# Kernel optimization log

Measured on AMD Instinct MI355X. Metric: run time of the kernel, lower is better.

## Reference

```python
import jax, jax.numpy as jnp
import numpy as np

NUM_GROUPS = 32
NUM_HEADS = 8
EPS = 1e-6


def group_norm(x, gamma, beta):
    B, C, H, W = x.shape
    xg = x.reshape(B, NUM_GROUPS, C // NUM_GROUPS, H, W)
    mean = xg.mean(axis=(2, 3, 4), keepdims=True)
    var = xg.var(axis=(2, 3, 4), keepdims=True)
    xn = (xg - mean) * jax.lax.rsqrt(var + EPS)
    xn = xn.reshape(B, C, H, W)
    return xn * gamma[None, :, None, None] + beta[None, :, None, None]


def setup_inputs() -> dict:
    key = jax.random.key(0)
    ks = jax.random.split(key, 3)
    B, C, H, W = 8, 512, 32, 32
    x = jax.random.normal(ks[0], (B, C, H, W), dtype=jnp.float32)
    # xavier_uniform for conv1x1: fan_in=C, fan_out per weight
    lim_qkv = float(np.sqrt(6.0 / (C + 3 * C)))
    w_qkv = jax.random.uniform(ks[1], (3 * C, C), minval=-lim_qkv, maxval=lim_qkv, dtype=jnp.float32)
    b_qkv = jnp.zeros((3 * C,), dtype=jnp.float32)
    lim_p = float(np.sqrt(6.0 / (C + C)))
    w_proj = jax.random.uniform(ks[2], (C, C), minval=-lim_p, maxval=lim_p, dtype=jnp.float32)
    b_proj = jnp.zeros((C,), dtype=jnp.float32)
    gamma = jnp.ones((C,), dtype=jnp.float32)
    beta = jnp.zeros((C,), dtype=jnp.float32)
    return {"x": x, "gamma": gamma, "beta": beta, "w_qkv": w_qkv, "b_qkv": b_qkv,
            "w_proj": w_proj, "b_proj": b_proj}


def reference(x, gamma, beta, w_qkv, b_qkv, w_proj, b_proj):
    B, C, H, W = x.shape
    N = H * W
    hd = C // NUM_HEADS
    scale = hd ** -0.5

    x_norm = group_norm(x, gamma, beta)
    # conv1x1 == channel GEMM: (B,C,H,W) -> (B,3C,H,W)
    qkv = jnp.einsum('bchw,oc->bohw', x_norm, w_qkv) + b_qkv[None, :, None, None]
    qkv = qkv.reshape(B, 3, NUM_HEADS, hd, N).transpose(1, 0, 2, 4, 3)
    q, k, v = qkv[0], qkv[1], qkv[2]

    attn = jnp.einsum('bhnd,bhmd->bhnm', q, k) * scale
    attn = jax.nn.softmax(attn, axis=-1)
    out = jnp.einsum('bhnm,bhmd->bhnd', attn, v)

    out = out.transpose(0, 1, 3, 2).reshape(B, C, H, W)
    out = jnp.einsum('bchw,oc->bohw', out, w_proj) + b_proj[None, :, None, None]
    return x + out
```

## Files before the change

### kernel.cpp

```cpp
#include <hip/hip_runtime.h>

#define LOG2E 1.4426950408889634f

typedef short bf16x8 __attribute__((ext_vector_type(8)));
typedef short short4v __attribute__((ext_vector_type(4)));
typedef float f32x4 __attribute__((ext_vector_type(4)));
typedef _Float16 half4v __attribute__((ext_vector_type(4)));
typedef unsigned u32x4 __attribute__((ext_vector_type(4)));
typedef unsigned __attribute__((address_space(1))) u32g;
typedef unsigned __attribute__((address_space(3))) u32l;

#define MFMA16(a, b, c) __builtin_amdgcn_mfma_f32_16x16x32_bf16((a), (b), (c), 0, 0, 0)

__device__ __forceinline__ short f2bf(float f) {
  unsigned u = __builtin_bit_cast(unsigned, f);
  u += 0x7FFFu + ((u >> 16) & 1u);
  return (short)(u >> 16);
}

__device__ __forceinline__ unsigned cvtpk(float lo, float hi) {
  unsigned r;
  asm("v_cvt_pk_bf16_f32 %0, %1, %2" : "=v"(r) : "v"(lo), "v"(hi));
  return r;
}

__device__ __forceinline__ void g2l16(void* lds, const void* g) {
  __builtin_amdgcn_global_load_lds((u32g*)const_cast<void*>(g), (u32l*)lds, 16, 0, 0);
}

__global__ __launch_bounds__(256) void gn_kernel(const float* __restrict__ x,
                                                 const float* __restrict__ gamma,
                                                 const float* __restrict__ beta,
                                                 short* __restrict__ xn_t) {
  __shared__ _Float16 xs[16 * 1024];
  __shared__ float red[8];
  const int bg = blockIdx.x;
  const int b = bg >> 5, g = bg & 31;
  const int t = threadIdx.x;
  const float4* gx4 = (const float4*)(x + (size_t)(b * 512 + g * 16) * 1024);
  float s1 = 0.f, s2 = 0.f;
  for (int i = 0; i < 16; ++i) {
    float4 v = gx4[t + 256 * i];
    s1 += (v.x + v.y) + (v.z + v.w);
    s2 += (v.x * v.x + v.y * v.y) + (v.z * v.z + v.w * v.w);
    half4v pk = {(_Float16)v.x, (_Float16)v.y, (_Float16)v.z, (_Float16)v.w};
    *(half4v*)((char*)xs + i * 2048 + ((8 * t) ^ ((i & 7) << 4))) = pk;
  }
  for (int m = 1; m < 64; m <<= 1) {
    s1 += __shfl_xor(s1, m);
    s2 += __shfl_xor(s2, m);
  }
  if ((t & 63) == 0) {
    red[(t >> 6) * 2] = s1;
    red[(t >> 6) * 2 + 1] = s2;
  }
  __syncthreads();
  s1 = (red[0] + red[2]) + (red[4] + red[6]);
  s2 = (red[1] + red[3]) + (red[5] + red[7]);
  const float mean = s1 * (1.f / 16384.f);
  const float var = s2 * (1.f / 16384.f) - mean * mean;
  const float rstd = rsqrtf(var + 1e-6f);
  const int ci = t & 15;
  const float ga = gamma[g * 16 + ci] * rstd;
  const float be = beta[g * 16 + ci] - mean * ga;
  short* dst = xn_t + (size_t)b * 1024 * 512 + g * 16 + ci;
  const int sw = (ci & 7) << 4;
  for (int i = 0; i < 64; ++i) {
    int n = (t >> 4) + 16 * i;
    float v = (float)*(const _Float16*)((const char*)xs + ci * 2048 + ((2 * n) ^ sw));
    dst[(size_t)n * 512] = f2bf(fmaf(v, ga, be));
  }
}

__global__ __launch_bounds__(256) void f2bf2_kernel(const float* __restrict__ s1,
                                                    short* __restrict__ d1, int n1,
                                                    const float* __restrict__ s2,
                                                    short* __restrict__ d2) {
  int i = blockIdx.x * 256 + threadIdx.x;
  const float* s = (i < n1) ? s1 : s2;
  short* d = (i < n1) ? d1 : d2;
  int j = (i < n1) ? i : i - n1;
  float4 v = ((const float4*)s)[j];
  short4v o = {f2bf(v.x), f2bf(v.y), f2bf(v.z), f2bf(v.w)};
  *(short4v*)(d + (size_t)j * 4) = o;
}

__global__ __launch_bounds__(256) void qkv_gemm(const short* __restrict__ W,
                                                const short* __restrict__ xn,
                                                const float* __restrict__ bias,
                                                short* __restrict__ qbuf,
                                                short* __restrict__ kbuf,
                                                short* __restrict__ vtbuf) {
  __shared__ short a_sm[2][128 * 32];
  __shared__ short b_sm[2][128 * 32];
  const int t = threadIdx.x;
  const int lane = t & 63, w = t >> 6;
  const int nbase = blockIdx.x * 128;
  const int mbase = blockIdx.y * 128;
  const int b = blockIdx.z;
  const short* Asrc = W + (size_t)mbase * 512;
  const short* Bsrc = xn + (size_t)b * 1024 * 512 + (size_t)nbase * 512;

  const int j0 = t, j1 = t + 256;
  const int r0 = j0 >> 2, c0 = ((j0 & 3) ^ ((j0 >> 3) & 3)) * 8;
  const int r1 = j1 >> 2, c1 = ((j1 & 3) ^ ((j1 >> 3) & 3)) * 8;

#define STAGE(bi, kt)                                                 \
  {                                                                   \
    const int k0s = (kt) * 32;                                        \
    g2l16(&a_sm[bi][j0 * 8], Asrc + (size_t)r0 * 512 + k0s + c0);     \
    g2l16(&a_sm[bi][j1 * 8], Asrc + (size_t)r1 * 512 + k0s + c1);     \
    g2l16(&b_sm[bi][j0 * 8], Bsrc + (size_t)r0 * 512 + k0s + c0);     \
    g2l16(&b_sm[bi][j1 * 8], Bsrc + (size_t)r1 * 512 + k0s + c1);     \
  }

  const int wm = (w >> 1) * 64, wn = (w & 1) * 64;
  const int col = lane & 15, rg = lane >> 4;

  f32x4 acc[4][4] = {};

  STAGE(0, 0)
  __syncthreads();
  int cur = 0;

  for (int kt = 0; kt < 16; ++kt) {
    if (kt < 15) STAGE(cur ^ 1, kt + 1);
    bf16x8 af[4], bfr[4];
#pragma unroll
    for (int mf = 0; mf < 4; ++mf) {
      const int row = wm + mf * 16 + col;
      af[mf] = *(const bf16x8*)&a_sm[cur][row * 32 + ((rg ^ ((row >> 1) & 3)) * 8)];
    }
#pragma unroll
    for (int nf = 0; nf < 4; ++nf) {
      const int row = wn + nf * 16 + col;
      bfr[nf] = *(const bf16x8*)&b_sm[cur][row * 32 + ((rg ^ ((row >> 1) & 3)) * 8)];
    }
    __builtin_amdgcn_s_setprio(1);
#pragma unroll
    for (int mf = 0; mf < 4; ++mf)
#pragma unroll
      for (int nf = 0; nf < 4; ++nf)
        acc[mf][nf] = MFMA16(af[mf], bfr[nf], acc[mf][nf]);
    __builtin_amdgcn_s_setprio(0);
    __syncthreads();
    cur ^= 1;
  }
#undef STAGE

  const int section = mbase >> 9;
  for (int mf = 0; mf < 4; ++mf) {
    const int o0 = mbase + wm + mf * 16 + rg * 4;
    const int h = (o0 >> 6) & 7, d0 = o0 & 63;
    float b4[4];
    for (int r = 0; r < 4; ++r) b4[r] = bias[o0 + r];
    for (int nf = 0; nf < 4; ++nf) {
      const int n = nbase + wn + nf * 16 + col;
      if (section < 2) {
        short4v pkv;
        for (int r = 0; r < 4; ++r) pkv[r] = f2bf(acc[mf][nf][r] + b4[r]);
        short* dst = (section == 0) ? qbuf : kbuf;
        *(short4v*)&dst[((size_t)(b * 8 + h) * 1024 + n) * 64 + d0] = pkv;
      } else {
        for (int r = 0; r < 4; ++r)
          vtbuf[((size_t)(b * 8 + h) * 64 + d0 + r) * 1024 + n] =
              f2bf(acc[mf][nf][r] + b4[r]);
      }
    }
  }
}

__global__ __launch_bounds__(512, 4) void attn_kernel(const short* __restrict__ qbuf,
                                                      const short* __restrict__ kbuf,
                                                      const short* __restrict__ vtbuf,
                                                      short* __restrict__ ao) {
  __shared__ char smem[65536];
  const int t = threadIdx.x, lane = t & 63, w = t >> 6;
  const int col = lane & 15, rg = lane >> 4;
  const int grp = w >> 2, wq = w & 3;
  const int tg = t & 255;
  const int bh = blockIdx.x, qt = blockIdx.y;
  const int b = bh >> 3, h = bh & 7;
  const int qbase = qt * 128 + wq * 32;

  short* kb_ = (short*)(smem + grp * 32768);
  short* vb_ = (short*)(smem + grp * 32768 + 16384);

  bf16x8 aq[2][2];
  {
    const short* qp = qbuf + ((size_t)bh * 1024 + qbase) * 64;
#pragma unroll
    for (int mf = 0; mf < 2; ++mf)
#pragma unroll
      for (int kc = 0; kc < 2; ++kc)
        aq[mf][kc] = *(const bf16x8*)&qp[(mf * 16 + col) * 64 + kc * 32 + rg * 8];
  }

  const short* kp0 = kbuf + (size_t)bh * 65536 + grp * 32768;
  const short* vp0 = vtbuf + (size_t)bh * 65536 + grp * 512;

  uint4 kr[2], vr[2];
#define LOADK(kt)                                                                  \
  _Pragma("unroll") for (int i = 0; i < 2; ++i) {                                  \
    int j = tg + 256 * i;                                                          \
    kr[i] = *(const uint4*)&kp0[((size_t)(kt)*64 + (j >> 3)) * 64 + (j & 7) * 8];  \
  }
#define LOADV(kt)                                                                  \
  _Pragma("unroll") for (int i = 0; i < 2; ++i) {                                  \
    int j = tg + 256 * i;                                                          \
    vr[i] = *(const uint4*)&vp0[(size_t)(j >> 3) * 1024 + (kt)*64 + (j & 7) * 8];  \
  }
#define WRITEK(bi)                                                                 \
  _Pragma("unroll") for (int i = 0; i < 2; ++i) {                                  \
    int j = tg + 256 * i;                                                          \
    int row = j >> 3, off = j & 7;                                                 \
    *(uint4*)((char*)kb_ + (bi)*8192 + row * 128 + ((off * 16) ^ ((row & 7) << 4))) = kr[i]; \
  }
#define WRITEV(bi)                                                                 \
  _Pragma("unroll") for (int i = 0; i < 2; ++i) {                                  \
    int j = tg + 256 * i;                                                          \
    int d = j >> 3, g = j & 7;                                                     \
    int base = (g >> 2) * 64 + (g & 1) * 32 + ((g >> 1) & 1) * 8;                  \
    char* vb = (char*)vb_ + (bi)*8192 + d * 128;                                   \
    uint2 lo = {vr[i].x, vr[i].y}, hi = {vr[i].z, vr[i].w};                        \
    *(uint2*)(vb + ((base) ^ ((d & 7) << 4))) = lo;                                \
    *(uint2*)(vb + ((base + 16) ^ ((d & 7) << 4))) = hi;                           \
  }

  f32x4 oacc[2][4] = {};
  float mrun[2] = {-3e38f, -3e38f}, lrun[2] = {0.f, 0.f};
  const float kSL2E = 0.125f * LOG2E;
  int cur = 0;

  LOADK(0) LOADV(0) WRITEK(0) WRITEV(0)
  __syncthreads();

  for (int kt = 0; kt < 8; ++kt) {
    if (kt < 7) { LOADK(kt + 1) LOADV(kt + 1) }

    f32x4 sT[2][4];
    __builtin_amdgcn_s_setprio(1);
#pragma unroll
    for (int nf = 0; nf < 4; ++nf) {
      const int n = nf * 16 + col;
      const char* kb = (const char*)kb_ + cur * 8192 + n * 128;
      const int sw = (n & 7) << 4;
      bf16x8 bk0 = *(const bf16x8*)(kb + ((rg * 16) ^ sw));
      bf16x8 bk1 = *(const bf16x8*)(kb + ((64 + rg * 16) ^ sw));
#pragma unroll
      for (int mf = 0; mf < 2; ++mf) {
        f32x4 z = {};
        z = MFMA16(bk0, aq[mf][0], z);
        sT[mf][nf] = MFMA16(bk1, aq[mf][1], z);
      }
    }
    __builtin_amdgcn_s_setprio(0);

    unsigned pk[2][4][2];
#pragma unroll
    for (int mf = 0; mf < 2; ++mf) {
      f32x4 mv = sT[mf][0];
#pragma unroll
      for (int nf = 1; nf < 4; ++nf)
#pragma unroll
        for (int r = 0; r < 4; ++r) mv[r] = fmaxf(mv[r], sT[mf][nf][r]);
      float mx = fmaxf(fmaxf(mv[0], mv[1]), fmaxf(mv[2], mv[3]));
      if (!__all(mx * 0.125f <= mrun[mf] + 8.f)) {
        float mxr = fmaxf(mx, __shfl_xor(mx, 16));
        mxr = fmaxf(mxr, __shfl_xor(mxr, 32));
        const float pmax = mxr * 0.125f;
        const float mnew = fmaxf(mrun[mf], pmax);
        const float alpha = __builtin_amdgcn_exp2f((mrun[mf] - mnew) * LOG2E);
        mrun[mf] = mnew;
        lrun[mf] *= alpha;
#pragma unroll
        for (int df = 0; df < 4; ++df) oacc[mf][df] *= alpha;
      }
      const float nege = mrun[mf] * LOG2E;
      float psum = 0.f;
#pragma unroll
      for (int nf = 0; nf < 4; ++nf) {
        float p0 = __builtin_amdgcn_exp2f(fmaf(sT[mf][nf][0], kSL2E, -nege));
        float p1 = __builtin_amdgcn_exp2f(fmaf(sT[mf][nf][1], kSL2E, -nege));
        float p2 = __builtin_amdgcn_exp2f(fmaf(sT[mf][nf][2], kSL2E, -nege));
        float p3 = __builtin_amdgcn_exp2f(fmaf(sT[mf][nf][3], kSL2E, -nege));
        psum += (p0 + p1) + (p2 + p3);
        pk[mf][nf][0] = cvtpk(p0, p1);
        pk[mf][nf][1] = cvtpk(p2, p3);
      }
      lrun[mf] += psum;
    }

    __builtin_amdgcn_s_setprio(1);
#pragma unroll
    for (int kc = 0; kc < 2; ++kc) {
      bf16x8 pb[2];
#pragma unroll
      for (int mf = 0; mf < 2; ++mf) {
        u32x4 pbu = {pk[mf][2 * kc][0], pk[mf][2 * kc][1], pk[mf][2 * kc + 1][0],
                     pk[mf][2 * kc + 1][1]};
        pb[mf] = __builtin_bit_cast(bf16x8, pbu);
      }
#pragma unroll
      for (int df = 0; df < 4; ++df) {
        const int d = df * 16 + col;
        bf16x8 av = *(const bf16x8*)((const char*)vb_ + cur * 8192 + d * 128 +
                                     ((kc * 64 + rg * 16) ^ ((d & 7) << 4)));
#pragma unroll
        for (int mf = 0; mf < 2; ++mf) oacc[mf][df] = MFMA16(av, pb[mf], oacc[mf][df]);
      }
    }
    __builtin_amdgcn_s_setprio(0);

    if (kt < 7) { WRITEK(cur ^ 1) WRITEV(cur ^ 1) }
    __syncthreads();
    cur ^= 1;
  }

#pragma unroll
  for (int mf = 0; mf < 2; ++mf) {
    float l = lrun[mf];
    l += __shfl_xor(l, 16);
    l += __shfl_xor(l, 32);
    lrun[mf] = l;
  }

  f32x4* o_lds = (f32x4*)smem;
  float* ml_lds = (float*)(smem + 32768);
  if (grp == 1) {
#pragma unroll
    for (int mf = 0; mf < 2; ++mf) {
#pragma unroll
      for (int df = 0; df < 4; ++df)
        o_lds[(((wq * 2 + mf) * 4) + df) * 64 + lane] = oacc[mf][df];
      ml_lds[((wq * 2 + mf) * 64 + lane) * 2] = mrun[mf];
      ml_lds[((wq * 2 + mf) * 64 + lane) * 2 + 1] = lrun[mf];
    }
  }
  __syncthreads();
  if (grp == 0) {
#pragma unroll
    for (int mf = 0; mf < 2; ++mf) {
      const float m1 = ml_lds[((wq * 2 + mf) * 64 + lane) * 2];
      const float l1 = ml_lds[((wq * 2 + mf) * 64 + lane) * 2 + 1];
      const float m = fmaxf(mrun[mf], m1);
      const float a0 = __builtin_amdgcn_exp2f((mrun[mf] - m) * LOG2E);
      const float a1 = __builtin_amdgcn_exp2f((m1 - m) * LOG2E);
      const float rl = 1.f / (lrun[mf] * a0 + l1 * a1);
      const int q = qbase + mf * 16 + col;
      short* dst = ao + ((size_t)b * 1024 + q) * 512 + h * 64;
#pragma unroll
      for (int df = 0; df < 4; ++df) {
        f32x4 o1 = o_lds[(((wq * 2 + mf) * 4) + df) * 64 + lane];
        short4v pkv;
#pragma unroll
        for (int r = 0; r < 4; ++r)
          pkv[r] = f2bf((oacc[mf][df][r] * a0 + o1[r] * a1) * rl);
        *(short4v*)&dst[df * 16 + rg * 4] = pkv;
      }
    }
  }
#undef LOADK
#undef LOADV
#undef WRITEK
#undef WRITEV
}

__global__ __launch_bounds__(256) void proj_gemm(const short* __restrict__ W,
                                                 const short* __restrict__ ao,
                                                 const float* __restrict__ bias,
                                                 const float* __restrict__ x,
                                                 float* __restrict__ out) {
  __shared__ short a_sm[2][64 * 32];
  __shared__ short b_sm[2][128 * 32];
  const int t = threadIdx.x;
  const int lane = t & 63, w = t >> 6;
  const int nbase = blockIdx.x * 128;
  const int mbase = blockIdx.y * 64;
  const int b = blockIdx.z;
  const short* Asrc = W + (size_t)mbase * 512;
  const short* Bsrc = ao + (size_t)b * 1024 * 512 + (size_t)nbase * 512;

  const int j0 = t, j1 = t + 256;
  const int r0 = j0 >> 2, c0 = ((j0 & 3) ^ ((j0 >> 3) & 3)) * 8;
  const int r1 = j1 >> 2, c1 = ((j1 & 3) ^ ((j1 >> 3) & 3)) * 8;

#define STAGE(bi, kt)                                                 \
  {                                                                   \
    const int k0s = (kt) * 32;                                        \
    g2l16(&a_sm[bi][j0 * 8], Asrc + (size_t)r0 * 512 + k0s + c0);     \
    g2l16(&b_sm[bi][j0 * 8], Bsrc + (size_t)r0 * 512 + k0s + c0);     \
    g2l16(&b_sm[bi][j1 * 8], Bsrc + (size_t)r1 * 512 + k0s + c1);     \
  }

  const int wm = (w >> 1) * 32, wn = (w & 1) * 64;
  const int col = lane & 15, rg = lane >> 4;

  f32x4 acc[2][4] = {};

  STAGE(0, 0)
  __syncthreads();
  int cur = 0;

  for (int kt = 0; kt < 16; ++kt) {
    if (kt < 15) STAGE(cur ^ 1, kt + 1);
    bf16x8 af[2], bfr[4];
#pragma unroll
    for (int mf = 0; mf < 2; ++mf) {
      const int row = wm + mf * 16 + col;
      af[mf] = *(const bf16x8*)&a_sm[cur][row * 32 + ((rg ^ ((row >> 1) & 3)) * 8)];
    }
#pragma unroll
    for (int nf = 0; nf < 4; ++nf) {
      const int row = wn + nf * 16 + col;
      bfr[nf] = *(const bf16x8*)&b_sm[cur][row * 32 + ((rg ^ ((row >> 1) & 3)) * 8)];
    }
    __builtin_amdgcn_s_setprio(1);
#pragma unroll
    for (int mf = 0; mf < 2; ++mf)
#pragma unroll
      for (int nf = 0; nf < 4; ++nf)
        acc[mf][nf] = MFMA16(af[mf], bfr[nf], acc[mf][nf]);
    __builtin_amdgcn_s_setprio(0);
    __syncthreads();
    cur ^= 1;
  }
#undef STAGE

  for (int mf = 0; mf < 2; ++mf) {
    const int o0 = mbase + wm + mf * 16 + rg * 4;
    float b4[4];
    for (int r = 0; r < 4; ++r) b4[r] = bias[o0 + r];
    for (int nf = 0; nf < 4; ++nf) {
      const int n = nbase + wn + nf * 16 + col;
      for (int r = 0; r < 4; ++r) {
        size_t idx = ((size_t)b * 512 + o0 + r) * 1024 + n;
        out[idx] = x[idx] + acc[mf][nf][r] + b4[r];
      }
    }
  }
}

extern "C" void kernel_launch(void* const* d_in, const int* in_sizes, int n_in,
                              void* d_out, int out_size, void* d_ws, size_t ws_size,
                              hipStream_t stream) {
  const float* x = (const float*)d_in[0];
  const float* gamma = (const float*)d_in[1];
  const float* beta = (const float*)d_in[2];
  const float* w_qkv = (const float*)d_in[3];
  const float* b_qkv = (const float*)d_in[4];
  const float* w_proj = (const float*)d_in[5];
  const float* b_proj = (const float*)d_in[6];
  float* out = (float*)d_out;

  char* ws = (char*)d_ws;
  short* xn_t = (short*)(ws);
  short* wqkv_b = (short*)(ws + 8388608);
  short* wproj_b = (short*)(ws + 9961472);
  short* qbuf = (short*)(ws + 10485760);
  short* kbuf = (short*)(ws + 18874368);
  short* vtbuf = (short*)(ws + 27262976);
  short* aobuf = (short*)(ws + 35651584);

  gn_kernel<<<dim3(256), dim3(256), 0, stream>>>(x, gamma, beta, xn_t);
  f2bf2_kernel<<<dim3(1024), dim3(256), 0, stream>>>(w_qkv, wqkv_b, 196608, w_proj,
                                                     wproj_b);
  qkv_gemm<<<dim3(8, 12, 8), dim3(256), 0, stream>>>(wqkv_b, xn_t, b_qkv, qbuf, kbuf,
                                                     vtbuf);
  attn_kernel<<<dim3(64, 8), dim3(512), 0, stream>>>(qbuf, kbuf, vtbuf, aobuf);
  proj_gemm<<<dim3(8, 8, 8), dim3(256), 0, stream>>>(wproj_b, aobuf, b_proj, x, out);
}
```

Before: 76.65 us.

## Triple-buffer GEMM LDS staging with explicit vmcnt waits and single barrier

Both the QKV and projection GEMMs move from double to triple LDS buffering. Each iteration issues the next tile's async global-to-LDS loads, waits with a partial vmcnt so only the current tile's loads must have landed, then hits one barrier. This drops the second __syncthreads per iteration and lets global loads overlap the MFMA work. The cost is 50% more shared memory per block, which can lower occupancy, plus a dependence on exact vmcnt counting with hand-written waits.

```diff
diff --git a/kernel.cpp b/kernel.cpp
--- a/kernel.cpp
+++ b/kernel.cpp
@@ -91,8 +91,8 @@
                                                 short* __restrict__ qbuf,
                                                 short* __restrict__ kbuf,
                                                 short* __restrict__ vtbuf) {
-  __shared__ short a_sm[2][128 * 32];
-  __shared__ short b_sm[2][128 * 32];
+  __shared__ short a_sm[3][128 * 32];
+  __shared__ short b_sm[3][128 * 32];
   const int t = threadIdx.x;
   const int lane = t & 63, w = t >> 6;
   const int nbase = blockIdx.x * 128;
@@ -120,11 +120,18 @@
   f32x4 acc[4][4] = {};
 
   STAGE(0, 0)
-  __syncthreads();
-  int cur = 0;
+  int cur = 0, nxt = 1;
 
   for (int kt = 0; kt < 16; ++kt) {
-    if (kt < 15) STAGE(cur ^ 1, kt + 1);
+    if (kt < 15) {
+      STAGE(nxt, kt + 1)
+      asm volatile("s_waitcnt vmcnt(4)" ::: "memory");
+    } else {
+      asm volatile("s_waitcnt vmcnt(0)" ::: "memory");
+    }
+    __builtin_amdgcn_s_barrier();
+    __builtin_amdgcn_sched_barrier(0);
+
     bf16x8 af[4], bfr[4];
 #pragma unroll
     for (int mf = 0; mf < 4; ++mf) {
@@ -143,8 +150,8 @@
       for (int nf = 0; nf < 4; ++nf)
         acc[mf][nf] = MFMA16(af[mf], bfr[nf], acc[mf][nf]);
     __builtin_amdgcn_s_setprio(0);
-    __syncthreads();
-    cur ^= 1;
+    cur = nxt;
+    nxt = (nxt == 2) ? 0 : nxt + 1;
   }
 #undef STAGE
 
@@ -371,8 +378,8 @@
                                                  const float* __restrict__ bias,
                                                  const float* __restrict__ x,
                                                  float* __restrict__ out) {
-  __shared__ short a_sm[2][64 * 32];
-  __shared__ short b_sm[2][128 * 32];
+  __shared__ short a_sm[3][64 * 32];
+  __shared__ short b_sm[3][128 * 32];
   const int t = threadIdx.x;
   const int lane = t & 63, w = t >> 6;
   const int nbase = blockIdx.x * 128;
@@ -399,11 +406,18 @@
   f32x4 acc[2][4] = {};
 
   STAGE(0, 0)
-  __syncthreads();
-  int cur = 0;
+  int cur = 0, nxt = 1;
 
   for (int kt = 0; kt < 16; ++kt) {
-    if (kt < 15) STAGE(cur ^ 1, kt + 1);
+    if (kt < 15) {
+      STAGE(nxt, kt + 1)
+      asm volatile("s_waitcnt vmcnt(3)" ::: "memory");
+    } else {
+      asm volatile("s_waitcnt vmcnt(0)" ::: "memory");
+    }
+    __builtin_amdgcn_s_barrier();
+    __builtin_amdgcn_sched_barrier(0);
+
     bf16x8 af[2], bfr[4];
 #pragma unroll
     for (int mf = 0; mf < 2; ++mf) {
@@ -422,8 +436,8 @@
       for (int nf = 0; nf < 4; ++nf)
         acc[mf][nf] = MFMA16(af[mf], bfr[nf], acc[mf][nf]);
     __builtin_amdgcn_s_setprio(0);
-    __syncthreads();
-    cur ^= 1;
+    cur = nxt;
+    nxt = (nxt == 2) ? 0 : nxt + 1;
   }
 #undef STAGE
 
```

Measured after the change: 75.57 us. Within noise of the previous version (-1.4%).
